# Kernel optimization log

Measured on AMD Instinct MI355X. Metric: run time of the kernel, lower is better.

Reference implementation:

```python
import jax, jax.numpy as jnp
import numpy as np


def conv1x1(x, w, b):
    # x: [B,C,H,W], w: [O,C], b: [O] -> [B,O,H,W]
    return jnp.einsum('bchw,oc->bohw', x, w) + b[None, :, None, None]


def setup_inputs() -> dict:
    key = jax.random.key(0)
    ks = jax.random.split(key, 8)
    B, C, H, W = 16, 256, 64, 64
    Cq = C // 8
    x = jax.random.normal(ks[0], (B, C, H, W), dtype=jnp.float32)
    wq = jax.random.normal(ks[1], (Cq, C), dtype=jnp.float32) * (2.0 / C) ** 0.5
    bq = jnp.zeros((Cq,), dtype=jnp.float32)
    wk = jax.random.normal(ks[2], (Cq, C), dtype=jnp.float32) * (2.0 / C) ** 0.5
    bk = jnp.zeros((Cq,), dtype=jnp.float32)
    wv = jax.random.normal(ks[3], (C, C), dtype=jnp.float32) * (2.0 / C) ** 0.5
    bv = jnp.zeros((C,), dtype=jnp.float32)
    gamma = jax.random.normal(ks[4], (1,), dtype=jnp.float32) * 0.1
    return {'x': x, 'wq': wq, 'bq': bq, 'wk': wk, 'bk': bk, 'wv': wv, 'bv': bv, 'gamma': gamma}


def reference(x, wq, bq, wk, bk, wv, bv, gamma):
    B, C, H, W = x.shape
    bH = B // 4
    bW = B // 4  # requires bH*bW == B, i.e. B == 16
    q = conv1x1(x, wq, bq)   # [B, C/8, H, W]
    k = conv1x1(x, wk, bk)   # [B, C/8, H, W]
    v = conv1x1(x, wv, bv)   # [B, C, H, W]
    # batch index b -> grid (h = b // bW, w = b % bW); token feature = flat map
    qg = q.reshape(bH, bW, -1)  # [bH, bW, Dq]
    kg = k.reshape(bH, bW, -1)
    vg = v.reshape(bH, bW, -1)  # [bH, bW, Dv]
    # column ('H') attention with -inf diagonal, row ('W') attention
    eH = jnp.einsum('hwd,gwd->hwg', qg, kg)  # [bH, bW, bH]
    eye = jnp.eye(bH, dtype=bool)[:, None, :]  # mask h == h'
    eH = jnp.where(eye, -jnp.inf, eH)
    eW = jnp.einsum('hwd,hgd->hwg', qg, kg)  # [bH, bW, bW]
    att = jax.nn.softmax(jnp.concatenate([eH, eW], axis=-1), axis=-1)
    aH, aW = att[..., :bH], att[..., bH:]
    oH = jnp.einsum('hwg,gwd->hwd', aH, vg)  # attend down the column
    oW = jnp.einsum('hwg,hgd->hwd', aW, vg)  # attend along the row
    out = (oH + oW).reshape(B, C, H, W)
    return gamma[0] * out + x
```

## Files before the change

### kernel.cpp

```cpp
#include <hip/hip_runtime.h>

#define HW_  4096
#define DQK  131072
#define DV   1048576

using bf16x8 = __attribute__((ext_vector_type(8))) __bf16;
using f32x4  = __attribute__((ext_vector_type(4))) float;

static __device__ __forceinline__ unsigned short f2bf(float f) {
    union { float f; unsigned u; } v; v.f = f;
    unsigned r = v.u + 0x7FFFu + ((v.u >> 16) & 1u);
    return (unsigned short)(r >> 16);
}
static __device__ __forceinline__ float bf2f(unsigned short h) {
    union { unsigned u; float f; } v; v.u = ((unsigned)h) << 16;
    return v.f;
}

__global__ __launch_bounds__(256) void k_pack(const float* wq, const float* wk, const float* wv,
                                              unsigned short* WhF, unsigned short* WlF, unsigned short* WvF) {
    int idx = blockIdx.x * 256 + threadIdx.x;
    if (idx < 16384) {
        int i = idx;
        int mt = i >> 12, cg = (i >> 7) & 31, ml = (i >> 3) & 15, cl = i & 7;
        int m = mt * 16 + ml, c = cg * 8 + cl;
        float f = (m < 32) ? wq[m * 256 + c] : wk[(m - 32) * 256 + c];
        unsigned short hi = f2bf(f);
        WhF[i] = hi;
        WlF[i] = f2bf(f - bf2f(hi));
    } else {
        int i = idx - 16384;
        int mt = i >> 12, kt = (i >> 7) & 31, lr = (i >> 3) & 15, j = i & 7;
        int m = mt * 16 + lr, c = kt * 8 + j;
        WvF[i] = f2bf(wv[m * 256 + c]);
    }
}

__global__ __launch_bounds__(256) void k_gemm_qk(const unsigned short* __restrict__ WhF,
                                                 const unsigned short* __restrict__ WlF,
                                                 const float* __restrict__ x,
                                                 const float* __restrict__ bq, const float* __restrict__ bk,
                                                 float* __restrict__ QF, float* __restrict__ KF) {
    int b  = blockIdx.y;
    int n0 = blockIdx.x * 64;
    int t = threadIdx.x;
    int lane = t & 63, wid = t >> 6;
    int wm = wid & 1, wn = wid >> 1;
    int lr = lane & 15, kg = lane >> 4;

    const float* xb = x + (size_t)b * DV;
    const unsigned short* Ah0 = WhF + (size_t)(wm * 2) * 4096 + lane * 8;
    const unsigned short* Al0 = WlF + (size_t)(wm * 2) * 4096 + lane * 8;

    f32x4 acc[2][2];
    for (int mi = 0; mi < 2; mi++)
        for (int ni = 0; ni < 2; ni++) acc[mi][ni] = (f32x4){0.f, 0.f, 0.f, 0.f};

    for (int kk = 0; kk < 8; kk++) {
        bf16x8 ah[2], al[2];
        for (int mi = 0; mi < 2; mi++) {
            ah[mi] = *(const bf16x8*)(Ah0 + (size_t)mi * 4096 + kk * 512);
            al[mi] = *(const bf16x8*)(Al0 + (size_t)mi * 4096 + kk * 512);
        }
        bf16x8 bh[2], bl[2];
        int cbase = kk * 32 + kg * 8;
        for (int ni = 0; ni < 2; ni++) {
            const float* xp = xb + (size_t)cbase * HW_ + n0 + wn * 32 + ni * 16 + lr;
            #pragma unroll
            for (int j = 0; j < 8; j++) {
                float v = xp[(size_t)j * HW_];
                __bf16 h = (__bf16)v;
                bh[ni][j] = h;
                bl[ni][j] = (__bf16)(v - (float)h);
            }
        }
        for (int mi = 0; mi < 2; mi++)
            for (int ni = 0; ni < 2; ni++) {
                acc[mi][ni] = __builtin_amdgcn_mfma_f32_16x16x32_bf16(ah[mi], bh[ni], acc[mi][ni], 0, 0, 0);
                acc[mi][ni] = __builtin_amdgcn_mfma_f32_16x16x32_bf16(ah[mi], bl[ni], acc[mi][ni], 0, 0, 0);
                acc[mi][ni] = __builtin_amdgcn_mfma_f32_16x16x32_bf16(al[mi], bh[ni], acc[mi][ni], 0, 0, 0);
            }
    }

    float* dst = (wm == 0) ? QF : KF;
    const float* bias = (wm == 0) ? bq : bk;
    for (int mi = 0; mi < 2; mi++) {
        int mq0 = mi * 16 + kg * 4;
        for (int i = 0; i < 4; i++) {
            int mq = mq0 + i;
            float bs = bias[mq];
            for (int ni = 0; ni < 2; ni++) {
                int n = n0 + wn * 32 + ni * 16 + lr;
                dst[(size_t)b * DQK + (size_t)mq * HW_ + n] = acc[mi][ni][i] + bs;
            }
        }
    }
}

__global__ __launch_bounds__(256) void k_scores2(const float* __restrict__ QF, const float* __restrict__ KF,
                                                 float* __restrict__ Sp) {
    __shared__ float Ql[16][520], Kl[16][520];
    int s = blockIdx.x;
    int m = s >> 3, off = (s & 7) * 512;
    int t = threadIdx.x;
    for (int b = 0; b < 16; b++) {
        const float* qs = QF + (size_t)b * DQK + (size_t)m * HW_ + off;
        const float* ks = KF + (size_t)b * DQK + (size_t)m * HW_ + off;
        Ql[b][t]       = qs[t];
        Ql[b][t + 256] = qs[t + 256];
        Kl[b][t]       = ks[t];
        Kl[b][t + 256] = ks[t + 256];
    }
    __syncthreads();
    int p = t >> 1, h = t & 1;
    int b = p >> 3, j = p & 7;
    int hb = b >> 2, wb = b & 3;
    int bp = (j < 4) ? (j * 4 + wb) : (hb * 4 + (j - 4));
    const f32x4* q4 = (const f32x4*)&Ql[b][h * 256];
    const f32x4* k4 = (const f32x4*)&Kl[bp][h * 256];
    f32x4 a4 = (f32x4){0.f, 0.f, 0.f, 0.f};
    for (int i = 0; i < 64; i++) a4 += q4[i] * k4[i];
    float sres = a4[0] + a4[1] + a4[2] + a4[3];
    sres += __shfl_xor(sres, 1);
    if (h == 0) Sp[(size_t)p * 256 + s] = sres;
}

__global__ void k_softmax2(const float* __restrict__ Sp, const float* __restrict__ gamma,
                           float* __restrict__ Mm) {
    __shared__ float SS[128];
    int t = threadIdx.x;
    const f32x4* s4 = (const f32x4*)(Sp + (size_t)t * 256);
    f32x4 a = (f32x4){0.f, 0.f, 0.f, 0.f};
    for (int i = 0; i < 64; i++) a += s4[i];
    SS[t] = a[0] + a[1] + a[2] + a[3];
    __syncthreads();
    if (t < 16) {
        int b = t, h = b >> 2, w = b & 3;
        float e[8];
        for (int j = 0; j < 8; j++) e[j] = SS[b * 8 + j];
        e[h] = -INFINITY;
        float mx = e[0];
        for (int j = 1; j < 8; j++) mx = fmaxf(mx, e[j]);
        float aa[8], sum = 0.f;
        for (int j = 0; j < 8; j++) { aa[j] = expf(e[j] - mx); sum += aa[j]; }
        float inv = 1.0f / sum;
        float g = gamma[0];
        float row[16];
        for (int c = 0; c < 16; c++) row[c] = 0.f;
        for (int gg = 0; gg < 4; gg++) if (gg != h) row[gg * 4 + w] += aa[gg] * inv;
        for (int gg = 0; gg < 4; gg++) row[h * 4 + gg] += aa[4 + gg] * inv;
        for (int c = 0; c < 16; c++) Mm[b * 16 + c] = row[c] * g;
        Mm[256 + b] = g;
    }
}

__global__ __launch_bounds__(1024, 4) void k_fused(const unsigned short* __restrict__ WvF,
                                                   const float* __restrict__ x,
                                                   const float* __restrict__ bv,
                                                   const float* __restrict__ Mm,
                                                   float* __restrict__ out) {
    __shared__ __align__(16) __bf16 XB[2][16][1088];
    int n0 = blockIdx.x * 16;
    int t = threadIdx.x;
    int lane = t & 63, wid = t >> 6;
    int lr = lane & 15, kg = lane >> 4;
    int n4 = t & 3, sk = (t >> 2) & 63, bpg = t >> 8;
    int sigr = ((lr & 3) << 2) | (lr >> 2);

    f32x4 u[16];
    #pragma unroll
    for (int b = 0; b < 16; b++) u[b] = (f32x4){0.f, 0.f, 0.f, 0.f};

    f32x4 xv[4];
    #pragma unroll
    for (int bpi = 0; bpi < 4; bpi++)
        xv[bpi] = *(const f32x4*)(x + (size_t)(bpg * 4 + bpi) * DV + (size_t)sk * HW_ + n0 + n4 * 4);
    {
        int rowoff = (sk >> 3) * 136 + (sk & 7);
        #pragma unroll
        for (int bpi = 0; bpi < 4; bpi++) {
            __bf16* basep = &XB[0][bpg * 4 + bpi][rowoff];
            #pragma unroll
            for (int e = 0; e < 4; e++)
                basep[((e << 2) | n4) * 8] = (__bf16)xv[bpi][e];
        }
    }
    __syncthreads();

    for (int c = 0; c < 4; c++) {
        int cur = c & 1;
        if (c < 3) {
            #pragma unroll
            for (int bpi = 0; bpi < 4; bpi++)
                xv[bpi] = *(const f32x4*)(x + (size_t)(bpg * 4 + bpi) * DV + (size_t)((c + 1) * 64 + sk) * HW_ + n0 + n4 * 4);
        }
        #pragma unroll
        for (int sub = 0; sub < 2; sub++) {
            bf16x8 a = *(const bf16x8*)(WvF + (size_t)wid * 4096 + (c * 2 + sub) * 512 + lane * 8);
            const __bf16* bbase = &XB[cur][0][(sub * 4 + kg) * 136 + sigr * 8];
            #pragma unroll
            for (int bp = 0; bp < 16; bp++) {
                bf16x8 bb = *(const bf16x8*)(bbase + bp * 1088);
                u[bp] = __builtin_amdgcn_mfma_f32_16x16x32_bf16(a, bb, u[bp], 0, 0, 0);
            }
        }
        if (c < 3) {
            int nb = cur ^ 1;
            int rowoff = (sk >> 3) * 136 + (sk & 7);
            #pragma unroll
            for (int bpi = 0; bpi < 4; bpi++) {
                __bf16* basep = &XB[nb][bpg * 4 + bpi][rowoff];
                #pragma unroll
                for (int e = 0; e < 4; e++)
                    basep[((e << 2) | n4) * 8] = (__bf16)xv[bpi][e];
            }
        }
        __syncthreads();
    }

    int mrow0 = wid * 16 + kg * 4;
    f32x4 bv4 = (f32x4){bv[mrow0], bv[mrow0 + 1], bv[mrow0 + 2], bv[mrow0 + 3]};
    #pragma unroll
    for (int b = 0; b < 16; b++) {
        int h = b >> 2, w = b & 3;
        f32x4 mo = (f32x4){0.f, 0.f, 0.f, 0.f};
        #pragma unroll
        for (int g = 0; g < 4; g++) {
            if (g != h) mo += Mm[b * 16 + g * 4 + w] * u[g * 4 + w];
            mo += Mm[b * 16 + h * 4 + g] * u[h * 4 + g];
        }
        mo += Mm[256 + b] * bv4;
        #pragma unroll
        for (int i = 0; i < 4; i++) {
            size_t idx = (size_t)b * DV + (size_t)(mrow0 + i) * HW_ + n0 + lr;
            out[idx] = mo[i] + x[idx];
        }
    }
}

extern "C" void kernel_launch(void* const* d_in, const int* in_sizes, int n_in,
                              void* d_out, int out_size, void* d_ws, size_t ws_size,
                              hipStream_t stream) {
    (void)in_sizes; (void)n_in; (void)out_size; (void)ws_size;
    const float* x     = (const float*)d_in[0];
    const float* wq    = (const float*)d_in[1];
    const float* bq    = (const float*)d_in[2];
    const float* wk    = (const float*)d_in[3];
    const float* bk    = (const float*)d_in[4];
    const float* wv    = (const float*)d_in[5];
    const float* bv    = (const float*)d_in[6];
    const float* gamma = (const float*)d_in[7];

    char* ws = (char*)d_ws;
    unsigned short* WhF = (unsigned short*)(ws + 0);
    unsigned short* WlF = (unsigned short*)(ws + 32768);
    unsigned short* WvF = (unsigned short*)(ws + 65536);
    float*          QF  = (float*)(ws + 196608);
    float*          KF  = (float*)(ws + 8585216);
    float*          Sp  = (float*)(ws + 16973824);
    float*          Mm  = (float*)(ws + 17104896);
    float*          vo  = (float*)d_out;

    k_pack     <<<320, 256, 0, stream>>>(wq, wk, wv, WhF, WlF, WvF);
    k_gemm_qk  <<<dim3(64, 16), 256, 0, stream>>>(WhF, WlF, x, bq, bk, QF, KF);
    k_scores2  <<<256, 256, 0, stream>>>(QF, KF, Sp);
    k_softmax2 <<<1, 128, 0, stream>>>(Sp, gamma, Mm);
    k_fused    <<<256, 1024, 0, stream>>>(WvF, x, bv, Mm, vo);
}
```

Before: 92.91 us.

## Split fused value GEMM across two output-channel halves and vectorize epilogue stores

The fused value-projection kernel now launches 512-thread blocks on a 2D grid, each block covering half of the 256 output channels. This doubles the block count and shrinks per-block size, but each block still loads and converts the full x tile, so x staging is done twice. The epilogue uses a 4x4 lane transpose built from cross-lane shuffles. That lets each lane issue one 16-byte load of the residual x and one 16-byte store of out, instead of four scalar accesses.

Result: slower. 102.6 us (+10.4%).

```diff
diff --git a/kernel.cpp b/kernel.cpp
--- a/kernel.cpp
+++ b/kernel.cpp
@@ -15,6 +15,26 @@
 static __device__ __forceinline__ float bf2f(unsigned short h) {
     union { unsigned u; float f; } v; v.u = ((unsigned)h) << 16;
     return v.f;
+}
+
+static __device__ __forceinline__ f32x4 xp4(f32x4 v, bool p0, bool p1) {
+    float e01 = p0 ? v[0] : v[1];
+    float r01 = __shfl_xor(e01, 1);
+    float x0 = p0 ? r01 : v[0];
+    float x1 = p0 ? v[1] : r01;
+    float e23 = p0 ? v[2] : v[3];
+    float r23 = __shfl_xor(e23, 1);
+    float x2 = p0 ? r23 : v[2];
+    float x3 = p0 ? v[3] : r23;
+    float eA = p1 ? x0 : x2;
+    float rA = __shfl_xor(eA, 2);
+    float w0 = p1 ? rA : x0;
+    float w2 = p1 ? x2 : rA;
+    float eB = p1 ? x1 : x3;
+    float rB = __shfl_xor(eB, 2);
+    float w1 = p1 ? rB : x1;
+    float w3 = p1 ? x3 : rB;
+    return (f32x4){w0, w1, w2, w3};
 }
 
 __global__ __launch_bounds__(256) void k_pack(const float* wq, const float* wk, const float* wv,
@@ -154,13 +174,14 @@
     }
 }
 
-__global__ __launch_bounds__(1024, 4) void k_fused(const unsigned short* __restrict__ WvF,
-                                                   const float* __restrict__ x,
-                                                   const float* __restrict__ bv,
-                                                   const float* __restrict__ Mm,
-                                                   float* __restrict__ out) {
+__global__ __launch_bounds__(512, 4) void k_fused(const unsigned short* __restrict__ WvF,
+                                                  const float* __restrict__ x,
+                                                  const float* __restrict__ bv,
+                                                  const float* __restrict__ Mm,
+                                                  float* __restrict__ out) {
     __shared__ __align__(16) __bf16 XB[2][16][1088];
     int n0 = blockIdx.x * 16;
+    int mhalf = blockIdx.y;
     int t = threadIdx.x;
     int lane = t & 63, wid = t >> 6;
     int lr = lane & 15, kg = lane >> 4;
@@ -171,32 +192,34 @@
     #pragma unroll
     for (int b = 0; b < 16; b++) u[b] = (f32x4){0.f, 0.f, 0.f, 0.f};
 
-    f32x4 xv[4];
+    f32x4 xv[8];
     #pragma unroll
-    for (int bpi = 0; bpi < 4; bpi++)
-        xv[bpi] = *(const f32x4*)(x + (size_t)(bpg * 4 + bpi) * DV + (size_t)sk * HW_ + n0 + n4 * 4);
+    for (int bpi = 0; bpi < 8; bpi++)
+        xv[bpi] = *(const f32x4*)(x + (size_t)(bpg * 8 + bpi) * DV + (size_t)sk * HW_ + n0 + n4 * 4);
     {
         int rowoff = (sk >> 3) * 136 + (sk & 7);
         #pragma unroll
-        for (int bpi = 0; bpi < 4; bpi++) {
-            __bf16* basep = &XB[0][bpg * 4 + bpi][rowoff];
+        for (int bpi = 0; bpi < 8; bpi++) {
+            __bf16* basep = &XB[0][bpg * 8 + bpi][rowoff];
             #pragma unroll
             for (int e = 0; e < 4; e++)
                 basep[((e << 2) | n4) * 8] = (__bf16)xv[bpi][e];
         }
     }
     __syncthreads();
+
+    const unsigned short* Wvb = WvF + (size_t)(mhalf * 8 + wid) * 4096 + lane * 8;
 
     for (int c = 0; c < 4; c++) {
         int cur = c & 1;
         if (c < 3) {
             #pragma unroll
-            for (int bpi = 0; bpi < 4; bpi++)
-                xv[bpi] = *(const f32x4*)(x + (size_t)(bpg * 4 + bpi) * DV + (size_t)((c + 1) * 64 + sk) * HW_ + n0 + n4 * 4);
+            for (int bpi = 0; bpi < 8; bpi++)
+                xv[bpi] = *(const f32x4*)(x + (size_t)(bpg * 8 + bpi) * DV + (size_t)((c + 1) * 64 + sk) * HW_ + n0 + n4 * 4);
         }
         #pragma unroll
         for (int sub = 0; sub < 2; sub++) {
-            bf16x8 a = *(const bf16x8*)(WvF + (size_t)wid * 4096 + (c * 2 + sub) * 512 + lane * 8);
+            bf16x8 a = *(const bf16x8*)(Wvb + (c * 2 + sub) * 512);
             const __bf16* bbase = &XB[cur][0][(sub * 4 + kg) * 136 + sigr * 8];
             #pragma unroll
             for (int bp = 0; bp < 16; bp++) {
@@ -208,8 +231,8 @@
             int nb = cur ^ 1;
             int rowoff = (sk >> 3) * 136 + (sk & 7);
             #pragma unroll
-            for (int bpi = 0; bpi < 4; bpi++) {
-                __bf16* basep = &XB[nb][bpg * 4 + bpi][rowoff];
+            for (int bpi = 0; bpi < 8; bpi++) {
+                __bf16* basep = &XB[nb][bpg * 8 + bpi][rowoff];
                 #pragma unroll
                 for (int e = 0; e < 4; e++)
                     basep[((e << 2) | n4) * 8] = (__bf16)xv[bpi][e];
@@ -218,8 +241,11 @@
         __syncthreads();
     }
 
-    int mrow0 = wid * 16 + kg * 4;
+    int mrow0 = mhalf * 128 + wid * 16 + kg * 4;
     f32x4 bv4 = (f32x4){bv[mrow0], bv[mrow0 + 1], bv[mrow0 + 2], bv[mrow0 + 3]};
+    bool p0 = (lane & 1) != 0, p1 = (lane & 2) != 0;
+    int mrow = mrow0 + (lane & 3);
+    int nq = n0 + (lr >> 2) * 4;
     #pragma unroll
     for (int b = 0; b < 16; b++) {
         int h = b >> 2, w = b & 3;
@@ -230,11 +256,10 @@
             mo += Mm[b * 16 + h * 4 + g] * u[h * 4 + g];
         }
         mo += Mm[256 + b] * bv4;
-        #pragma unroll
-        for (int i = 0; i < 4; i++) {
-            size_t idx = (size_t)b * DV + (size_t)(mrow0 + i) * HW_ + n0 + lr;
-            out[idx] = mo[i] + x[idx];
-        }
+        f32x4 wv4 = xp4(mo, p0, p1);
+        size_t gidx = (size_t)b * DV + (size_t)mrow * HW_ + nq;
+        f32x4 rr = *(const f32x4*)(x + gidx);
+        *(f32x4*)(out + gidx) = wv4 + rr;
     }
 }
 
@@ -265,5 +290,5 @@
     k_gemm_qk  <<<dim3(64, 16), 256, 0, stream>>>(WhF, WlF, x, bq, bk, QF, KF);
     k_scores2  <<<256, 256, 0, stream>>>(QF, KF, Sp);
     k_softmax2 <<<1, 128, 0, stream>>>(Sp, gamma, Mm);
-    k_fused    <<<256, 1024, 0, stream>>>(WvF, x, bv, Mm, vo);
-}
+    k_fused    <<<dim3(256, 2), 512, 0, stream>>>(WvF, x, bv, Mm, vo);
+}
```
